# Kernel tuning notes

Measured on AMD Instinct MI355X. Metric: run time of the kernel, lower is better.

Reference implementation:

```python
import jax, jax.numpy as jnp
import numpy as np

VOCAB = 100000
EMB = 300
B, L = 2048, 256

def setup_inputs() -> dict:
    key = jax.random.key(0)
    k1, k2, k3, k4 = jax.random.split(key, 4)
    tokens = jax.random.randint(k1, (B, L), 0, VOCAB)
    # lengths in [1, L] (original items always have at least one token)
    lengths = jax.random.randint(k2, (B,), 1, L + 1)
    W_emb = jax.random.normal(k3, (VOCAB, EMB), dtype=jnp.float32)
    fc_w = jax.random.normal(k4, (1, EMB), dtype=jnp.float32) / np.sqrt(EMB)
    fc_b = jnp.zeros((1,), dtype=jnp.float32)
    return {"tokens": tokens, "lengths": lengths, "W_emb": W_emb, "fc_w": fc_w, "fc_b": fc_b}

def reference(tokens, lengths, W_emb, fc_w, fc_b):
    # ragged gather + per-item mean pool, fused via padding mask
    emb = W_emb[tokens]                                   # [B, L, D]
    mask = (jnp.arange(L)[None, :] < lengths[:, None])    # [B, L]
    summed = jnp.einsum('bld,bl->bd', emb, mask.astype(emb.dtype))
    avg = summed / lengths[:, None].astype(emb.dtype)     # [B, D]
    z = avg @ fc_w.T + fc_b                               # [B, 1]
    return jax.nn.sigmoid(z)
```

## Files before the change

kernel.cpp:

```cpp
#include <hip/hip_runtime.h>
#include <hip/hip_bf16.h>

#define VOCAB 100000
#define EMB 300
#define BATCH 2048
#define SEQ 256

typedef float f4 __attribute__((ext_vector_type(4)));

__global__ void __launch_bounds__(256) vocab_dot_kernel(
    const float* __restrict__ W, const float* __restrict__ fcw,
    float* __restrict__ p, int nrows) {
  const int lane = threadIdx.x & 63;
  const int g    = lane >> 4;
  const int i    = lane & 15;
  const int wave = (blockIdx.x * blockDim.x + threadIdx.x) >> 6;
  const int nwaves = (gridDim.x * blockDim.x) >> 6;

  const f4* fcw4 = (const f4*)fcw;
  const f4 zero = {0.f, 0.f, 0.f, 0.f};
  f4 w0 = fcw4[i];
  f4 w1 = fcw4[i + 16];
  f4 w2 = fcw4[i + 32];
  f4 w3 = fcw4[i + 48];
  f4 w4 = (i < 11) ? fcw4[i + 64] : zero;

  for (int v0 = wave * 4; v0 < nrows; v0 += nwaves * 4) {
    const int v = v0 + g;
    float acc = 0.f;
    if (v < nrows) {
      const f4* r = (const f4*)(W + (size_t)v * EMB);
      f4 a0 = r[i];
      f4 a1 = r[i + 16];
      f4 a2 = r[i + 32];
      f4 a3 = r[i + 48];
      f4 a4 = (i < 11) ? r[i + 64] : zero;
      f4 s = a0 * w0 + a1 * w1 + a2 * w2 + a3 * w3 + a4 * w4;
      acc = s.x + s.y + s.z + s.w;
    }
    acc += __shfl_xor(acc, 8, 16);
    acc += __shfl_xor(acc, 4, 16);
    acc += __shfl_xor(acc, 2, 16);
    acc += __shfl_xor(acc, 1, 16);
    if (i == 0 && v < nrows) p[v] = acc;
  }
}

__global__ void __launch_bounds__(256) pool_sigmoid_kernel(
    const int* __restrict__ tokens, const int* __restrict__ lengths,
    const float* __restrict__ p, const float* __restrict__ fcb,
    float* __restrict__ out, int L) {
  __shared__ float part[4];
  const int b = blockIdx.x;
  const int t = threadIdx.x;
  const int len = lengths[b];

  float acc = 0.f;
  if (t < len) acc = p[tokens[(size_t)b * L + t]];

  #pragma unroll
  for (int off = 32; off > 0; off >>= 1)
    acc += __shfl_down(acc, off, 64);

  const int lane = t & 63, w = t >> 6;
  if (lane == 0) part[w] = acc;
  __syncthreads();
  if (t == 0) {
    float s = part[0] + part[1] + part[2] + part[3];
    float z = s / (float)len + fcb[0];
    out[b] = 1.0f / (1.0f + expf(-z));
  }
}

extern "C" void kernel_launch(void* const* d_in, const int* in_sizes, int n_in,
                              void* d_out, int out_size, void* d_ws, size_t ws_size,
                              hipStream_t stream) {
  const int*   tokens  = (const int*)d_in[0];
  const int*   lengths = (const int*)d_in[1];
  const float* W_emb   = (const float*)d_in[2];
  const float* fc_w    = (const float*)d_in[3];
  const float* fc_b    = (const float*)d_in[4];
  float* out = (float*)d_out;
  float* p   = (float*)d_ws;

  vocab_dot_kernel<<<2048, 256, 0, stream>>>(W_emb, fc_w, p, VOCAB);

  pool_sigmoid_kernel<<<BATCH, 256, 0, stream>>>(
      tokens, lengths, p, fc_b, out, SEQ);
}
```

Measured before the change: 27.79 us.

## Use exact-cover grid with nontemporal loads and wave-per-item pooling

The vocab projection kernel now launches exactly enough blocks (3125×4 waves×8 rows = 100000) so each wave handles two rows with no grid-stride loop or bounds checks. Row loads use nontemporal hints and are issued together to raise memory-level parallelism. The pooling kernel assigns one wave per batch item, reads tokens as int4 vectors and drops shared memory and __syncthreads. The change relies on VOCAB being an exact multiple of 32 and has no tail handling.

After: 26.68 us. -4.0%, faster.

```diff
diff --git a/kernel.cpp b/kernel.cpp
--- a/kernel.cpp
+++ b/kernel.cpp
@@ -5,17 +5,18 @@
 #define EMB 300
 #define BATCH 2048
 #define SEQ 256
+#define NBLK1 3125
 
 typedef float f4 __attribute__((ext_vector_type(4)));
+typedef int   i4 __attribute__((ext_vector_type(4)));
 
 __global__ void __launch_bounds__(256) vocab_dot_kernel(
     const float* __restrict__ W, const float* __restrict__ fcw,
-    float* __restrict__ p, int nrows) {
+    float* __restrict__ p) {
   const int lane = threadIdx.x & 63;
   const int g    = lane >> 4;
   const int i    = lane & 15;
-  const int wave = (blockIdx.x * blockDim.x + threadIdx.x) >> 6;
-  const int nwaves = (gridDim.x * blockDim.x) >> 6;
+  const int wave = (blockIdx.x * 256 + threadIdx.x) >> 6;
 
   const f4* fcw4 = (const f4*)fcw;
   const f4 zero = {0.f, 0.f, 0.f, 0.f};
@@ -25,49 +26,65 @@
   f4 w3 = fcw4[i + 48];
   f4 w4 = (i < 11) ? fcw4[i + 64] : zero;
 
-  for (int v0 = wave * 4; v0 < nrows; v0 += nwaves * 4) {
-    const int v = v0 + g;
-    float acc = 0.f;
-    if (v < nrows) {
-      const f4* r = (const f4*)(W + (size_t)v * EMB);
-      f4 a0 = r[i];
-      f4 a1 = r[i + 16];
-      f4 a2 = r[i + 32];
-      f4 a3 = r[i + 48];
-      f4 a4 = (i < 11) ? r[i + 64] : zero;
-      f4 s = a0 * w0 + a1 * w1 + a2 * w2 + a3 * w3 + a4 * w4;
-      acc = s.x + s.y + s.z + s.w;
-    }
-    acc += __shfl_xor(acc, 8, 16);
-    acc += __shfl_xor(acc, 4, 16);
-    acc += __shfl_xor(acc, 2, 16);
-    acc += __shfl_xor(acc, 1, 16);
-    if (i == 0 && v < nrows) p[v] = acc;
+  const int v0 = wave * 8 + g;
+  const int v1 = v0 + 4;
+  const f4* r0 = (const f4*)(W + (size_t)v0 * EMB);
+  const f4* r1 = (const f4*)(W + (size_t)v1 * EMB);
+
+  f4 a0 = __builtin_nontemporal_load(&r0[i]);
+  f4 a1 = __builtin_nontemporal_load(&r0[i + 16]);
+  f4 a2 = __builtin_nontemporal_load(&r0[i + 32]);
+  f4 a3 = __builtin_nontemporal_load(&r0[i + 48]);
+  f4 a4 = (i < 11) ? __builtin_nontemporal_load(&r0[i + 64]) : zero;
+  f4 b0 = __builtin_nontemporal_load(&r1[i]);
+  f4 b1 = __builtin_nontemporal_load(&r1[i + 16]);
+  f4 b2 = __builtin_nontemporal_load(&r1[i + 32]);
+  f4 b3 = __builtin_nontemporal_load(&r1[i + 48]);
+  f4 b4 = (i < 11) ? __builtin_nontemporal_load(&r1[i + 64]) : zero;
+
+  f4 s0 = a0 * w0 + a1 * w1 + a2 * w2 + a3 * w3 + a4 * w4;
+  f4 s1 = b0 * w0 + b1 * w1 + b2 * w2 + b3 * w3 + b4 * w4;
+  float acc0 = s0.x + s0.y + s0.z + s0.w;
+  float acc1 = s1.x + s1.y + s1.z + s1.w;
+
+  acc0 += __shfl_xor(acc0, 8, 16);
+  acc1 += __shfl_xor(acc1, 8, 16);
+  acc0 += __shfl_xor(acc0, 4, 16);
+  acc1 += __shfl_xor(acc1, 4, 16);
+  acc0 += __shfl_xor(acc0, 2, 16);
+  acc1 += __shfl_xor(acc1, 2, 16);
+  acc0 += __shfl_xor(acc0, 1, 16);
+  acc1 += __shfl_xor(acc1, 1, 16);
+  if (i == 0) {
+    p[v0] = acc0;
+    p[v1] = acc1;
   }
 }
 
 __global__ void __launch_bounds__(256) pool_sigmoid_kernel(
     const int* __restrict__ tokens, const int* __restrict__ lengths,
     const float* __restrict__ p, const float* __restrict__ fcb,
-    float* __restrict__ out, int L) {
-  __shared__ float part[4];
-  const int b = blockIdx.x;
-  const int t = threadIdx.x;
+    float* __restrict__ out) {
+  const int lane = threadIdx.x & 63;
+  const int w    = threadIdx.x >> 6;
+  const int b    = blockIdx.x * 4 + w;
+
   const int len = lengths[b];
+  const i4 t = ((const i4*)(tokens + (size_t)b * SEQ))[lane];
+  const int base = lane * 4;
 
   float acc = 0.f;
-  if (t < len) acc = p[tokens[(size_t)b * L + t]];
+  if (base + 0 < len) acc += p[t[0]];
+  if (base + 1 < len) acc += p[t[1]];
+  if (base + 2 < len) acc += p[t[2]];
+  if (base + 3 < len) acc += p[t[3]];
 
   #pragma unroll
   for (int off = 32; off > 0; off >>= 1)
     acc += __shfl_down(acc, off, 64);
 
-  const int lane = t & 63, w = t >> 6;
-  if (lane == 0) part[w] = acc;
-  __syncthreads();
-  if (t == 0) {
-    float s = part[0] + part[1] + part[2] + part[3];
-    float z = s / (float)len + fcb[0];
+  if (lane == 0) {
+    const float z = acc / (float)len + fcb[0];
     out[b] = 1.0f / (1.0f + expf(-z));
   }
 }
@@ -83,8 +100,8 @@
   float* out = (float*)d_out;
   float* p   = (float*)d_ws;
 
-  vocab_dot_kernel<<<2048, 256, 0, stream>>>(W_emb, fc_w, p, VOCAB);
+  vocab_dot_kernel<<<NBLK1, 256, 0, stream>>>(W_emb, fc_w, p);
 
-  pool_sigmoid_kernel<<<BATCH, 256, 0, stream>>>(
-      tokens, lengths, p, fc_b, out, SEQ);
+  pool_sigmoid_kernel<<<BATCH / 4, 256, 0, stream>>>(
+      tokens, lengths, p, fc_b, out);
 }
```
